# Kernel optimization log

Hardware: AMD Instinct MI355X
Metric: run time of the kernel (lower is better)

The kernel has to match this reference:

```python
import jax, jax.numpy as jnp
import numpy as np

B, T, C, H, E, K = 4, 2048, 512, 2048, 8, 2


def setup_inputs() -> dict:
    key = jax.random.key(0)
    ks = jax.random.split(key, 7)
    s_r = 1.0 / np.sqrt(C)
    s_h = 1.0 / np.sqrt(H)
    return {
        "x": jax.random.normal(ks[0], (B, T, C), dtype=jnp.float32),
        "Wr": jax.random.uniform(ks[1], (C, E), jnp.float32, -s_r, s_r),
        "br": jax.random.uniform(ks[2], (E,), jnp.float32, -s_r, s_r),
        "W1": jax.random.uniform(ks[3], (E, C, H), jnp.float32, -s_r, s_r),
        "b1": jax.random.uniform(ks[4], (E, H), jnp.float32, -s_r, s_r),
        "W2": jax.random.uniform(ks[5], (E, H, C), jnp.float32, -s_h, s_h),
        "b2": jax.random.uniform(ks[6], (E, C), jnp.float32, -s_h, s_h),
    }


def reference(x, Wr, br, W1, b1, W2, b2):
    # Router logits [B,T,E]
    logits = jnp.einsum("btc,ce->bte", x, Wr) + br
    topk_vals, topk_idx = jax.lax.top_k(logits, K)  # [B,T,K]
    scores = jax.nn.softmax(topk_vals, axis=-1)  # softmax over the K selected
    # Combine weights per expert: gate[b,t,e] = sum_k scores[b,t,k]*(idx==e)
    onehot = jax.nn.one_hot(topk_idx, E, dtype=x.dtype)  # [B,T,K,E]
    gate = jnp.einsum("btk,btke->bte", scores, onehot)  # [B,T,E]
    # Dense-masked expert MLPs (tokens not routed to e have gate==0)
    h = jax.nn.relu(jnp.einsum("btc,ech->bteh", x, W1) + b1)  # [B,T,E,H]
    y = jnp.einsum("bteh,ehc->btec", h, W2) + b2  # [B,T,E,C]
    out = jnp.einsum("btec,bte->btc", y, gate)  # weighted combine
    return logits, topk_idx, out
```

## Files before the change

### kernel.cpp

```cpp
#include <hip/hip_runtime.h>
#include <hip/hip_bf16.h>

#define NTOK 8192
#define NASN 16384
#define C_ 512
#define H_ 2048
#define E_ 8
#define RBC 2048

typedef __bf16 bf16x8 __attribute__((ext_vector_type(8)));
typedef float f32x4 __attribute__((ext_vector_type(4)));

#define WS_COUNTS 0
#define WS_OFFS   65536
#define WS_T1S    65792
#define WS_INFO   66048
#define WS_TOKL   (WS_INFO + NTOK*16)
#define WS_SLOTS  (WS_TOKL + NASN*4)
#define WS_XBF    (WS_SLOTS + NTOK*8)
#define WS_W1B    (WS_XBF + (size_t)NTOK*C_*2)
#define WS_W2B    (WS_W1B + (size_t)E_*H_*C_*2)
#define WS_HS     (WS_W2B + (size_t)E_*H_*C_*2)
#define WS_YS     WS_XBF

__device__ __forceinline__ unsigned int f2bf(float f) {
  __hip_bfloat16 h = __float2bfloat16(f);
  return (unsigned int)*(unsigned short*)&h;
}
__device__ __forceinline__ float bf2f(unsigned int u) {
  return __int_as_float((u & 0xffffu) << 16);
}

__device__ __forceinline__ void g2l16(const unsigned short* g, unsigned short* l) {
  __builtin_amdgcn_global_load_lds(
      (const __attribute__((address_space(1))) unsigned int*)g,
      (__attribute__((address_space(3))) unsigned int*)l, 16, 0, 0);
}

__device__ __forceinline__ void stage_decode(int L, int& brow, int& q) {
  int s = L >> 3, slot = L & 7;
  int v = slot ^ (s & 7);
  brow = 2*s + (v >> 2);
  q = v & 3;
}

__global__ __launch_bounds__(256) void k_fused(
    const float* __restrict__ x, const float* __restrict__ Wr,
    const float* __restrict__ br, float* __restrict__ out_logits,
    float* __restrict__ out_idx, int4* __restrict__ info,
    int* __restrict__ counts, unsigned short* __restrict__ Xbf,
    const float* __restrict__ W1, unsigned short* __restrict__ W1b,
    const float* __restrict__ W2, unsigned short* __restrict__ W2b)
{
  __shared__ float tileS[128][33];
  __shared__ int bc[8];
  int b = blockIdx.x;
  int tid = threadIdx.x;

  if (b < RBC) {
    if (tid < 8) bc[tid] = 0;
    __syncthreads();
    int t = b * 4 + (tid >> 6);
    int lane = tid & 63;
    const float4* xr = (const float4*)(x + (size_t)t * C_);
    float4 x0 = xr[lane*2], x1 = xr[lane*2+1];
    uint4 pk;
    pk.x = f2bf(x0.x) | (f2bf(x0.y) << 16);
    pk.y = f2bf(x0.z) | (f2bf(x0.w) << 16);
    pk.z = f2bf(x1.x) | (f2bf(x1.y) << 16);
    pk.w = f2bf(x1.z) | (f2bf(x1.w) << 16);
    *(uint4*)(Xbf + (size_t)t * C_ + lane*8) = pk;

    float xs[8] = {x0.x,x0.y,x0.z,x0.w,x1.x,x1.y,x1.z,x1.w};
    float acc[8] = {0,0,0,0,0,0,0,0};
    #pragma unroll
    for (int j = 0; j < 8; j++) {
      const float4* w = (const float4*)(Wr + (size_t)(lane*8+j) * E_);
      float4 w0 = w[0], w1 = w[1];
      float we[8] = {w0.x,w0.y,w0.z,w0.w,w1.x,w1.y,w1.z,w1.w};
      #pragma unroll
      for (int e = 0; e < 8; e++) acc[e] += xs[j] * we[e];
    }
    #pragma unroll
    for (int off = 1; off < 64; off <<= 1) {
      #pragma unroll
      for (int e = 0; e < 8; e++) acc[e] += __shfl_xor(acc[e], off, 64);
    }
    #pragma unroll
    for (int e = 0; e < 8; e++) acc[e] += br[e];
    if (lane == 0) {
      #pragma unroll
      for (int e = 0; e < 8; e++) out_logits[t*8 + e] = acc[e];
      int i0 = 0; float v0 = acc[0];
      #pragma unroll
      for (int e = 1; e < 8; e++) if (acc[e] > v0) { v0 = acc[e]; i0 = e; }
      int i1 = -1; float v1 = -1e30f;
      #pragma unroll
      for (int e = 0; e < 8; e++) if (e != i0 && acc[e] > v1) { v1 = acc[e]; i1 = e; }
      float d = expf(v1 - v0);
      float s1 = d / (1.0f + d);
      float s0 = 1.0f - s1;
      out_idx[t*2]     = (float)i0;
      out_idx[t*2 + 1] = (float)i1;
      info[t] = make_int4(i0, i1, __float_as_int(s0), __float_as_int(s1));
      atomicAdd(&bc[i0], 1);
      atomicAdd(&bc[i1], 1);
    }
    __syncthreads();
    if (tid < 8) counts[b*8 + tid] = bc[tid];
    return;
  }

  const float* in; unsigned short* outp; int R, S, bx, by, bz;
  if (b < 2*RBC) {
    int bb = b - RBC;
    in = W1; outp = W1b; R = C_; S = H_;
    bx = bb & 63; by = (bb >> 6) & 3; bz = bb >> 8;
  } else {
    int bb = b - 2*RBC;
    in = W2; outp = W2b; R = H_; S = C_;
    bx = bb & 15; by = (bb >> 4) & 15; bz = bb >> 8;
  }
  size_t zo = (size_t)bz * R * S;
  in += zo; outp += zo;
  int r0 = by * 128, s0 = bx * 32;
  #pragma unroll
  for (int i = 0; i < 16; i++) {
    int lin = i*256 + tid;
    int rr = lin >> 5, ss = lin & 31;
    tileS[rr][ss] = in[(size_t)(r0 + rr) * S + s0 + ss];
  }
  __syncthreads();
  #pragma unroll
  for (int i = 0; i < 4; i++) {
    int lin = i*256 + tid;
    int ss = lin >> 5, rq = lin & 31;
    ushort4 v;
    v.x = (unsigned short)f2bf(tileS[rq*4+0][ss]);
    v.y = (unsigned short)f2bf(tileS[rq*4+1][ss]);
    v.z = (unsigned short)f2bf(tileS[rq*4+2][ss]);
    v.w = (unsigned short)f2bf(tileS[rq*4+3][ss]);
    *(ushort4*)(outp + (size_t)(s0 + ss) * R + r0 + rq*4) = v;
  }
}

__global__ __launch_bounds__(64) void k_prefscatter(
    const int* __restrict__ counts, const int4* __restrict__ info,
    int* __restrict__ tokl, int2* __restrict__ slots2,
    int* __restrict__ offs, int* __restrict__ t1s)
{
  __shared__ int full_s[8][8];
  __shared__ int part_s[8][8];
  __shared__ int tot_s[8];
  __shared__ int off_s[9];
  __shared__ int cur[8];
  int c = blockIdx.x, t = threadIdx.x;
  int e = t & 7, g = t >> 3;
  int lim = c * 16;
  int full = 0, part = 0;
  for (int i = 0; i < 256; i++) {
    int rb = g*256 + i;
    int v = counts[rb*8 + e];
    full += v;
    if (rb < lim) part += v;
  }
  full_s[e][g] = full; part_s[e][g] = part;
  __syncthreads();
  if (t < 8) {
    int s = 0;
    #pragma unroll
    for (int gg = 0; gg < 8; gg++) s += full_s[t][gg];
    tot_s[t] = s;
  }
  __syncthreads();
  if (t == 0) {
    int o = 0;
    off_s[0] = 0;
    for (int ee = 0; ee < 8; ee++) { o += tot_s[ee]; off_s[ee+1] = o; }
    if (c == 0) {
      offs[0] = 0; t1s[0] = 0;
      int tt = 0;
      for (int ee = 0; ee < 8; ee++) {
        offs[ee+1] = off_s[ee+1];
        tt += (tot_s[ee] + 127) >> 7;
        t1s[ee+1] = tt;
      }
    }
  }
  __syncthreads();
  if (t < 8) {
    int mg = c >> 4;
    int bse = off_s[t];
    #pragma unroll
    for (int gg = 0; gg < 8; gg++) if (gg < mg) bse += full_s[t][gg];
    bse += part_s[t][mg];
    cur[t] = bse;
  }
  __syncthreads();
  int tok = c*64 + t;
  int4 nfo = info[tok];
  int r0 = atomicAdd(&cur[nfo.x], 1);
  int r1 = atomicAdd(&cur[nfo.y], 1);
  tokl[r0] = tok;
  tokl[r1] = tok;
  slots2[tok] = make_int2(r0, r1);
}

__global__ __launch_bounds__(256) void k_gemm1(
    const unsigned short* __restrict__ Xbf, const int* __restrict__ tokl,
    const unsigned short* __restrict__ W1b,
    const float* __restrict__ b1, unsigned short* __restrict__ Hs,
    const int* __restrict__ offs, const int* __restrict__ t1s)
{
  __shared__ __align__(16) unsigned short AB[2*8192];
  int b = blockIdx.x;
  int mo = b >> 7, rr = b & 127;
  int n0 = (rr >> 3) * 128;
  int mt = mo*8 + (rr & 7);
  if (mt >= t1s[8]) return;
  int e = 0;
  #pragma unroll
  for (int i = 0; i < 7; i++) if (mt >= t1s[e+1]) e++;
  int row0 = offs[e] + (mt - t1s[e]) * 128;
  int rowEnd = offs[e+1];
  int tid = threadIdx.x, lane = tid & 63, w = tid >> 6;
  int wm = (w & 1) * 64, wn = (w >> 1) * 64;
  int quad = lane >> 4, l16 = lane & 15;
  const f32x4 zero = {0.f, 0.f, 0.f, 0.f};
  f32x4 acc[4][4];
  #pragma unroll
  for (int i = 0; i < 4; i++)
    #pragma unroll
    for (int j = 0; j < 4; j++) acc[i][j] = zero;
  const unsigned short* Bsrc = W1b + ((size_t)e * H_ + n0) * C_;

  const unsigned short* ga[2]; const unsigned short* gb[2];
  int lao[2], lbo[2];
  #pragma unroll
  for (int j = 0; j < 2; j++) {
    int L = (w*2 + j)*64 + lane;
    int brow, q; stage_decode(L, brow, q);
    int gr = row0 + brow; gr = gr < NASN-1 ? gr : NASN-1;
    int trow = tokl[gr];
    ga[j] = Xbf + (size_t)trow * C_ + q*8;
    gb[j] = Bsrc + (size_t)brow * C_ + q*8;
    lao[j] = (w*2 + j)*512;
    lbo[j] = 4096 + (w*2 + j)*512;
  }
  int rbase = (l16>>1)*64 + ((((l16&1)<<2) + quad) ^ (l16>>1))*8;
  const int KI = C_ / 32;

  #pragma unroll
  for (int j = 0; j < 2; j++) { g2l16(ga[j], AB + lao[j]); g2l16(gb[j], AB + lbo[j]); }

  for (int ki = 0; ki < KI; ki++) {
    int p = ki & 1;
    if (ki + 1 < KI) {
      int off = (ki + 1) * 32;
      unsigned short* nb = AB + (p ^ 1) * 8192;
      #pragma unroll
      for (int j = 0; j < 2; j++) {
        g2l16(ga[j] + off, nb + lao[j]);
        g2l16(gb[j] + off, nb + lbo[j]);
      }
      asm volatile("s_waitcnt vmcnt(4)" ::: "memory");
    } else {
      asm volatile("s_waitcnt vmcnt(0)" ::: "memory");
    }
    asm volatile("s_barrier" ::: "memory");

    const unsigned short* Ap = AB + p*8192;
    const unsigned short* Bp = Ap + 4096;
    bf16x8 af[4], bfr[4];
    #pragma unroll
    for (int i = 0; i < 4; i++)
      af[i] = *(const bf16x8*)&Ap[wm*32 + i*512 + rbase];
    #pragma unroll
    for (int j = 0; j < 4; j++)
      bfr[j] = *(const bf16x8*)&Bp[wn*32 + j*512 + rbase];
    #pragma unroll
    for (int i = 0; i < 4; i++)
      #pragma unroll
      for (int j = 0; j < 4; j++)
        acc[i][j] = __builtin_amdgcn_mfma_f32_16x16x32_bf16(af[i], bfr[j], acc[i][j], 0, 0, 0);

    asm volatile("s_waitcnt lgkmcnt(0)" ::: "memory");
    asm volatile("s_barrier" ::: "memory");
  }

  unsigned short* Lt = AB + w*4096;
  #pragma unroll
  for (int j = 0; j < 4; j++) {
    int n = n0 + wn + j*16 + l16;
    float bias = b1[e * H_ + n];
    #pragma unroll
    for (int i = 0; i < 4; i++)
      #pragma unroll
      for (int r = 0; r < 4; r++) {
        float v = acc[i][j][r] + bias;
        Lt[(i*16 + quad*4 + r)*64 + j*16 + l16] = (unsigned short)f2bf(v > 0.f ? v : 0.f);
      }
  }
  #pragma unroll
  for (int it = 0; it < 8; it++) {
    int rloc = it*8 + (lane >> 3);
    int m = row0 + wm + rloc;
    uint4 vv = *(uint4*)&Lt[rloc*64 + (lane & 7)*8];
    if (m < rowEnd)
      *(uint4*)(Hs + (size_t)m * H_ + n0 + wn + (lane & 7)*8) = vv;
  }
}

__global__ __launch_bounds__(256) void k_gemm2(
    const unsigned short* __restrict__ Hs, const unsigned short* __restrict__ W2b,
    const float* __restrict__ b2, unsigned short* __restrict__ Ys,
    const int* __restrict__ offs, const int* __restrict__ t1s)
{
  __shared__ __align__(16) unsigned short AB[2*8192];
  int b = blockIdx.x;
  int mo = b >> 5, rr = b & 31;
  int n0 = (rr >> 3) * 128;
  int mt = mo*8 + (rr & 7);
  if (mt >= t1s[8]) return;
  int e = 0;
  #pragma unroll
  for (int i = 0; i < 7; i++) if (mt >= t1s[e+1]) e++;
  int row0 = offs[e] + (mt - t1s[e]) * 128;
  int rowEnd = offs[e+1];
  int tid = threadIdx.x, lane = tid & 63, w = tid >> 6;
  int wm = (w & 1) * 64, wn = (w >> 1) * 64;
  int quad = lane >> 4, l16 = lane & 15;
  const f32x4 zero = {0.f, 0.f, 0.f, 0.f};
  f32x4 acc[4][4];
  #pragma unroll
  for (int i = 0; i < 4; i++)
    #pragma unroll
    for (int j = 0; j < 4; j++) acc[i][j] = zero;
  const unsigned short* Bsrc = W2b + ((size_t)e * C_ + n0) * H_;

  const unsigned short* ga[2]; const unsigned short* gb[2];
  int lao[2], lbo[2];
  #pragma unroll
  for (int j = 0; j < 2; j++) {
    int L = (w*2 + j)*64 + lane;
    int brow, q; stage_decode(L, brow, q);
    int gr = row0 + brow; gr = gr < NASN-1 ? gr : NASN-1;
    ga[j] = Hs + (size_t)gr * H_ + q*8;
    gb[j] = Bsrc + (size_t)brow * H_ + q*8;
    lao[j] = (w*2 + j)*512;
    lbo[j] = 4096 + (w*2 + j)*512;
  }
  int rbase = (l16>>1)*64 + ((((l16&1)<<2) + quad) ^ (l16>>1))*8;
  const int KI = H_ / 32;

  #pragma unroll
  for (int j = 0; j < 2; j++) { g2l16(ga[j], AB + lao[j]); g2l16(gb[j], AB + lbo[j]); }

  for (int ki = 0; ki < KI; ki++) {
    int p = ki & 1;
    if (ki + 1 < KI) {
      int off = (ki + 1) * 32;
      unsigned short* nb = AB + (p ^ 1) * 8192;
      #pragma unroll
      for (int j = 0; j < 2; j++) {
        g2l16(ga[j] + off, nb + lao[j]);
        g2l16(gb[j] + off, nb + lbo[j]);
      }
      asm volatile("s_waitcnt vmcnt(4)" ::: "memory");
    } else {
      asm volatile("s_waitcnt vmcnt(0)" ::: "memory");
    }
    asm volatile("s_barrier" ::: "memory");

    const unsigned short* Ap = AB + p*8192;
    const unsigned short* Bp = Ap + 4096;
    bf16x8 af[4], bfr[4];
    #pragma unroll
    for (int i = 0; i < 4; i++)
      af[i] = *(const bf16x8*)&Ap[wm*32 + i*512 + rbase];
    #pragma unroll
    for (int j = 0; j < 4; j++)
      bfr[j] = *(const bf16x8*)&Bp[wn*32 + j*512 + rbase];
    #pragma unroll
    for (int i = 0; i < 4; i++)
      #pragma unroll
      for (int j = 0; j < 4; j++)
        acc[i][j] = __builtin_amdgcn_mfma_f32_16x16x32_bf16(af[i], bfr[j], acc[i][j], 0, 0, 0);

    asm volatile("s_waitcnt lgkmcnt(0)" ::: "memory");
    asm volatile("s_barrier" ::: "memory");
  }

  unsigned short* Lt = AB + w*4096;
  #pragma unroll
  for (int j = 0; j < 4; j++) {
    int n = n0 + wn + j*16 + l16;
    float bias = b2[e * C_ + n];
    #pragma unroll
    for (int i = 0; i < 4; i++)
      #pragma unroll
      for (int r = 0; r < 4; r++)
        Lt[(i*16 + quad*4 + r)*64 + j*16 + l16] =
            (unsigned short)f2bf(acc[i][j][r] + bias);
  }
  #pragma unroll
  for (int it = 0; it < 8; it++) {
    int rloc = it*8 + (lane >> 3);
    int m = row0 + wm + rloc;
    uint4 vv = *(uint4*)&Lt[rloc*64 + (lane & 7)*8];
    if (m < rowEnd)
      *(uint4*)(Ys + (size_t)m * C_ + n0 + wn + (lane & 7)*8) = vv;
  }
}

__global__ __launch_bounds__(256) void k_combine(
    const unsigned short* __restrict__ Ys, const int4* __restrict__ info,
    const int2* __restrict__ slots2, float* __restrict__ outp)
{
  int t = blockIdx.x * 4 + (threadIdx.x >> 6);
  int lane = threadIdx.x & 63;
  int4 nfo = info[t];
  int2 ss = slots2[t];
  float g0 = __int_as_float(nfo.z), g1 = __int_as_float(nfo.w);
  uint4 a = *(const uint4*)(Ys + (size_t)ss.x * C_ + lane*8);
  uint4 bb = *(const uint4*)(Ys + (size_t)ss.y * C_ + lane*8);
  unsigned int au[4] = {a.x, a.y, a.z, a.w};
  unsigned int bu[4] = {bb.x, bb.y, bb.z, bb.w};
  float vals[8];
  #pragma unroll
  for (int q = 0; q < 4; q++) {
    vals[q*2]   = g0*bf2f(au[q])       + g1*bf2f(bu[q]);
    vals[q*2+1] = g0*bf2f(au[q] >> 16) + g1*bf2f(bu[q] >> 16);
  }
  float4 o0, o1;
  o0.x = vals[0]; o0.y = vals[1]; o0.z = vals[2]; o0.w = vals[3];
  o1.x = vals[4]; o1.y = vals[5]; o1.z = vals[6]; o1.w = vals[7];
  float4* o = (float4*)(outp + (size_t)t * C_ + lane*8);
  o[0] = o0;
  o[1] = o1;
}

extern "C" void kernel_launch(void* const* d_in, const int* in_sizes, int n_in,
                              void* d_out, int out_size, void* d_ws, size_t ws_size,
                              hipStream_t stream)
{
  const float* x  = (const float*)d_in[0];
  const float* Wr = (const float*)d_in[1];
  const float* br = (const float*)d_in[2];
  const float* W1 = (const float*)d_in[3];
  const float* b1 = (const float*)d_in[4];
  const float* W2 = (const float*)d_in[5];
  const float* b2 = (const float*)d_in[6];
  float* out = (float*)d_out;
  char* ws = (char*)d_ws;

  int*  counts = (int*)(ws + WS_COUNTS);
  int*  offs   = (int*)(ws + WS_OFFS);
  int*  t1s    = (int*)(ws + WS_T1S);
  int4* info   = (int4*)(ws + WS_INFO);
  int*  tokl   = (int*)(ws + WS_TOKL);
  int2* slots2 = (int2*)(ws + WS_SLOTS);
  unsigned short* Xbf = (unsigned short*)(ws + WS_XBF);
  unsigned short* W1b = (unsigned short*)(ws + WS_W1B);
  unsigned short* W2b = (unsigned short*)(ws + WS_W2B);
  unsigned short* Hs  = (unsigned short*)(ws + WS_HS);
  unsigned short* Ys  = (unsigned short*)(ws + WS_YS);

  k_fused<<<3*RBC, 256, 0, stream>>>(x, Wr, br, out, out + 65536, info,
                                     counts, Xbf, W1, W1b, W2, W2b);
  k_prefscatter<<<128, 64, 0, stream>>>(counts, info, tokl, slots2, offs, t1s);
  k_gemm1<<<17*128, 256, 0, stream>>>(Xbf, tokl, W1b, b1, Hs, offs, t1s);
  k_gemm2<<<17*32, 256, 0, stream>>>(Hs, W2b, b2, Ys, offs, t1s);
  k_combine<<<NTOK/4, 256, 0, stream>>>(Ys, info, slots2, out + 81920);
}
```

Before: 274.0 us.

## Pre-swizzle weights into MFMA fragment layout and load B directly to registers

New measurement: 301.7 us. +10.1%, slower.

```diff
diff --git a/kernel.cpp b/kernel.cpp
--- a/kernel.cpp
+++ b/kernel.cpp
@@ -131,16 +131,28 @@
     tileS[rr][ss] = in[(size_t)(r0 + rr) * S + s0 + ss];
   }
   __syncthreads();
-  #pragma unroll
-  for (int i = 0; i < 4; i++) {
-    int lin = i*256 + tid;
-    int ss = lin >> 5, rq = lin & 31;
-    ushort4 v;
-    v.x = (unsigned short)f2bf(tileS[rq*4+0][ss]);
-    v.y = (unsigned short)f2bf(tileS[rq*4+1][ss]);
-    v.z = (unsigned short)f2bf(tileS[rq*4+2][ss]);
-    v.w = (unsigned short)f2bf(tileS[rq*4+3][ss]);
-    *(ushort4*)(outp + (size_t)(s0 + ss) * R + r0 + rq*4) = v;
+  {
+    int KId = R >> 5;
+    int g0 = s0 >> 4;
+    int sk0 = r0 >> 5;
+    int lane = tid & 63;
+    int l16 = lane & 15, quad = lane >> 4;
+    #pragma unroll
+    for (int pp = 0; pp < 2; pp++) {
+      int ch = pp*4 + (tid >> 6);
+      int gloc = ch >> 2, sloc = ch & 3;
+      unsigned short el[8];
+      #pragma unroll
+      for (int i = 0; i < 8; i++)
+        el[i] = (unsigned short)f2bf(tileS[sloc*32 + quad*8 + i][gloc*16 + l16]);
+      uint4 v;
+      v.x = (unsigned int)el[0] | ((unsigned int)el[1] << 16);
+      v.y = (unsigned int)el[2] | ((unsigned int)el[3] << 16);
+      v.z = (unsigned int)el[4] | ((unsigned int)el[5] << 16);
+      v.w = (unsigned int)el[6] | ((unsigned int)el[7] << 16);
+      size_t chunk = (size_t)(g0 + gloc) * KId + sk0 + sloc;
+      *(uint4*)((char*)outp + chunk*1024 + lane*16) = v;
+    }
   }
 }
 
@@ -206,13 +218,44 @@
   slots2[tok] = make_int2(r0, r1);
 }
 
+#define KSTEP(KIDX, BUSE, BLOAD)                                              \
+  {                                                                           \
+    int p_ = (KIDX) & 1;                                                      \
+    if ((KIDX) + 1 < KI) {                                                    \
+      int off_ = ((KIDX) + 1) * 32;                                           \
+      unsigned short* nb_ = AB + (p_ ^ 1) * 4096;                             \
+      _Pragma("unroll")                                                       \
+      for (int j = 0; j < 2; j++) g2l16(ga[j] + off_, nb_ + lao[j]);          \
+      _Pragma("unroll")                                                       \
+      for (int j = 0; j < 4; j++)                                             \
+        BLOAD[j] = *(const bf16x8*)(bp[j] + ((KIDX) + 1) * 1024);             \
+      asm volatile("s_waitcnt vmcnt(6)" ::: "memory");                        \
+    } else {                                                                  \
+      asm volatile("s_waitcnt vmcnt(0)" ::: "memory");                        \
+    }                                                                         \
+    asm volatile("s_barrier" ::: "memory");                                   \
+    const unsigned short* Ap_ = AB + p_ * 4096;                               \
+    bf16x8 af_[4];                                                            \
+    _Pragma("unroll")                                                         \
+    for (int i = 0; i < 4; i++)                                               \
+      af_[i] = *(const bf16x8*)&Ap_[wm*32 + i*512 + rbase];                   \
+    _Pragma("unroll")                                                         \
+    for (int i = 0; i < 4; i++)                                               \
+      _Pragma("unroll")                                                       \
+      for (int j = 0; j < 4; j++)                                             \
+        acc[i][j] = __builtin_amdgcn_mfma_f32_16x16x32_bf16(                  \
+            af_[i], BUSE[j], acc[i][j], 0, 0, 0);                             \
+    asm volatile("s_waitcnt lgkmcnt(0)" ::: "memory");                        \
+    asm volatile("s_barrier" ::: "memory");                                   \
+  }
+
 __global__ __launch_bounds__(256) void k_gemm1(
     const unsigned short* __restrict__ Xbf, const int* __restrict__ tokl,
     const unsigned short* __restrict__ W1b,
     const float* __restrict__ b1, unsigned short* __restrict__ Hs,
     const int* __restrict__ offs, const int* __restrict__ t1s)
 {
-  __shared__ __align__(16) unsigned short AB[2*8192];
+  __shared__ __align__(16) unsigned short AB[16384];
   int b = blockIdx.x;
   int mo = b >> 7, rr = b & 127;
   int n0 = (rr >> 3) * 128;
@@ -232,10 +275,8 @@
   for (int i = 0; i < 4; i++)
     #pragma unroll
     for (int j = 0; j < 4; j++) acc[i][j] = zero;
-  const unsigned short* Bsrc = W1b + ((size_t)e * H_ + n0) * C_;
-
-  const unsigned short* ga[2]; const unsigned short* gb[2];
-  int lao[2], lbo[2];
+
+  const unsigned short* ga[2]; int lao[2];
   #pragma unroll
   for (int j = 0; j < 2; j++) {
     int L = (w*2 + j)*64 + lane;
@@ -243,49 +284,28 @@
     int gr = row0 + brow; gr = gr < NASN-1 ? gr : NASN-1;
     int trow = tokl[gr];
     ga[j] = Xbf + (size_t)trow * C_ + q*8;
-    gb[j] = Bsrc + (size_t)brow * C_ + q*8;
     lao[j] = (w*2 + j)*512;
-    lbo[j] = 4096 + (w*2 + j)*512;
+  }
+  const char* bp[4];
+  {
+    const char* Bb = (const char*)W1b + (size_t)e * H_ * C_ * 2;
+    int g0w = (n0 + wn) >> 4;
+    #pragma unroll
+    for (int j = 0; j < 4; j++)
+      bp[j] = Bb + ((size_t)(g0w + j) * (C_/32)) * 1024 + lane*16;
   }
   int rbase = (l16>>1)*64 + ((((l16&1)<<2) + quad) ^ (l16>>1))*8;
   const int KI = C_ / 32;
 
   #pragma unroll
-  for (int j = 0; j < 2; j++) { g2l16(ga[j], AB + lao[j]); g2l16(gb[j], AB + lbo[j]); }
-
-  for (int ki = 0; ki < KI; ki++) {
-    int p = ki & 1;
-    if (ki + 1 < KI) {
-      int off = (ki + 1) * 32;
-      unsigned short* nb = AB + (p ^ 1) * 8192;
-      #pragma unroll
-      for (int j = 0; j < 2; j++) {
-        g2l16(ga[j] + off, nb + lao[j]);
-        g2l16(gb[j] + off, nb + lbo[j]);
-      }
-      asm volatile("s_waitcnt vmcnt(4)" ::: "memory");
-    } else {
-      asm volatile("s_waitcnt vmcnt(0)" ::: "memory");
-    }
-    asm volatile("s_barrier" ::: "memory");
-
-    const unsigned short* Ap = AB + p*8192;
-    const unsigned short* Bp = Ap + 4096;
-    bf16x8 af[4], bfr[4];
-    #pragma unroll
-    for (int i = 0; i < 4; i++)
-      af[i] = *(const bf16x8*)&Ap[wm*32 + i*512 + rbase];
-    #pragma unroll
-    for (int j = 0; j < 4; j++)
-      bfr[j] = *(const bf16x8*)&Bp[wn*32 + j*512 + rbase];
-    #pragma unroll
-    for (int i = 0; i < 4; i++)
-      #pragma unroll
-      for (int j = 0; j < 4; j++)
-        acc[i][j] = __builtin_amdgcn_mfma_f32_16x16x32_bf16(af[i], bfr[j], acc[i][j], 0, 0, 0);
-
-    asm volatile("s_waitcnt lgkmcnt(0)" ::: "memory");
-    asm volatile("s_barrier" ::: "memory");
+  for (int j = 0; j < 2; j++) g2l16(ga[j], AB + lao[j]);
+  bf16x8 bA[4], bB[4];
+  #pragma unroll
+  for (int j = 0; j < 4; j++) bA[j] = *(const bf16x8*)(bp[j]);
+
+  for (int ki = 0; ki < KI; ki += 2) {
+    KSTEP(ki,     bA, bB);
+    KSTEP(ki + 1, bB, bA);
   }
 
   unsigned short* Lt = AB + w*4096;
@@ -316,7 +336,7 @@
     const float* __restrict__ b2, unsigned short* __restrict__ Ys,
     const int* __restrict__ offs, const int* __restrict__ t1s)
 {
-  __shared__ __align__(16) unsigned short AB[2*8192];
+  __shared__ __align__(16) unsigned short AB[16384];
   int b = blockIdx.x;
   int mo = b >> 5, rr = b & 31;
   int n0 = (rr >> 3) * 128;
@@ -336,59 +356,36 @@
   for (int i = 0; i < 4; i++)
     #pragma unroll
     for (int j = 0; j < 4; j++) acc[i][j] = zero;
-  const unsigned short* Bsrc = W2b + ((size_t)e * C_ + n0) * H_;
-
-  const unsigned short* ga[2]; const unsigned short* gb[2];
-  int lao[2], lbo[2];
+
+  const unsigned short* ga[2]; int lao[2];
   #pragma unroll
   for (int j = 0; j < 2; j++) {
     int L = (w*2 + j)*64 + lane;
     int brow, q; stage_decode(L, brow, q);
     int gr = row0 + brow; gr = gr < NASN-1 ? gr : NASN-1;
     ga[j] = Hs + (size_t)gr * H_ + q*8;
-    gb[j] = Bsrc + (size_t)brow * H_ + q*8;
     lao[j] = (w*2 + j)*512;
-    lbo[j] = 4096 + (w*2 + j)*512;
+  }
+  const char* bp[4];
+  {
+    const char* Bb = (const char*)W2b + (size_t)e * C_ * H_ * 2;
+    int g0w = (n0 + wn) >> 4;
+    #pragma unroll
+    for (int j = 0; j < 4; j++)
+      bp[j] = Bb + ((size_t)(g0w + j) * (H_/32)) * 1024 + lane*16;
   }
   int rbase = (l16>>1)*64 + ((((l16&1)<<2) + quad) ^ (l16>>1))*8;
   const int KI = H_ / 32;
 
   #pragma unroll
-  for (int j = 0; j < 2; j++) { g2l16(ga[j], AB + lao[j]); g2l16(gb[j], AB + lbo[j]); }
-
-  for (int ki = 0; ki < KI; ki++) {
-    int p = ki & 1;
-    if (ki + 1 < KI) {
-      int off = (ki + 1) * 32;
-      unsigned short* nb = AB + (p ^ 1) * 8192;
-      #pragma unroll
-      for (int j = 0; j < 2; j++) {
-        g2l16(ga[j] + off, nb + lao[j]);
-        g2l16(gb[j] + off, nb + lbo[j]);
-      }
-      asm volatile("s_waitcnt vmcnt(4)" ::: "memory");
-    } else {
-      asm volatile("s_waitcnt vmcnt(0)" ::: "memory");
-    }
-    asm volatile("s_barrier" ::: "memory");
-
-    const unsigned short* Ap = AB + p*8192;
-    const unsigned short* Bp = Ap + 4096;
-    bf16x8 af[4], bfr[4];
-    #pragma unroll
-    for (int i = 0; i < 4; i++)
-      af[i] = *(const bf16x8*)&Ap[wm*32 + i*512 + rbase];
-    #pragma unroll
-    for (int j = 0; j < 4; j++)
-      bfr[j] = *(const bf16x8*)&Bp[wn*32 + j*512 + rbase];
-    #pragma unroll
-    for (int i = 0; i < 4; i++)
-      #pragma unroll
-      for (int j = 0; j < 4; j++)
-        acc[i][j] = __builtin_amdgcn_mfma_f32_16x16x32_bf16(af[i], bfr[j], acc[i][j], 0, 0, 0);
-
-    asm volatile("s_waitcnt lgkmcnt(0)" ::: "memory");
-    asm volatile("s_barrier" ::: "memory");
+  for (int j = 0; j < 2; j++) g2l16(ga[j], AB + lao[j]);
+  bf16x8 bA[4], bB[4];
+  #pragma unroll
+  for (int j = 0; j < 4; j++) bA[j] = *(const bf16x8*)(bp[j]);
+
+  for (int ki = 0; ki < KI; ki += 2) {
+    KSTEP(ki,     bA, bB);
+    KSTEP(ki + 1, bB, bA);
   }
 
   unsigned short* Lt = AB + w*4096;
```
